# Performance work log

Measured on AMD Instinct MI355X. Metric: run time of the kernel, lower is better.

The kernel has to match this reference:

```python
import jax, jax.numpy as jnp
import numpy as np

L = 96   # num_layers per GRU stack == seq_len (required by h0 construction in source)
B = 128  # batch
T = 96   # seq_len
D = 3    # input features (x,y,z landmark coords)


def _u(key, shape, s):
    return jax.random.uniform(key, shape, jnp.float32, minval=-s, maxval=s)


def setup_inputs() -> dict:
    key = jax.random.key(0)
    ks = iter(jax.random.split(key, 40))
    inp = {"x": jax.random.normal(next(ks), (B, T, D), jnp.float32)}

    def gru_params(pfx, din, h):
        s = 1.0 / np.sqrt(h).astype(np.float32)  # PyTorch GRU init scale
        inp[pfx + "_wih0"] = _u(next(ks), (3 * h, din), s)   # layer 0 input weights
        inp[pfx + "_bih0"] = _u(next(ks), (3 * h,), s)
        inp[pfx + "_whh0"] = _u(next(ks), (3 * h, h), s)
        inp[pfx + "_bhh0"] = _u(next(ks), (3 * h,), s)
        inp[pfx + "_wih"] = _u(next(ks), (L - 1, 3 * h, h), s)  # layers 1..L-1 (input dim == h)
        inp[pfx + "_bih"] = _u(next(ks), (L - 1, 3 * h), s)
        inp[pfx + "_whh"] = _u(next(ks), (L - 1, 3 * h, h), s)
        inp[pfx + "_bhh"] = _u(next(ks), (L - 1, 3 * h), s)

    gru_params("g1", D, 64)
    gru_params("g2", 64, 128)
    gru_params("g3", 128, 64)

    inp["d1_w"] = _u(next(ks), (64, 64), 1.0 / 8)
    inp["d1_b"] = _u(next(ks), (64,), 1.0 / 8)
    inp["d2_w"] = _u(next(ks), (32, 64), 1.0 / 8)
    inp["d2_b"] = _u(next(ks), (32,), 1.0 / 8)
    inp["d3_w"] = _u(next(ks), (250, 32), 1.0 / np.sqrt(32).astype(np.float32))
    inp["d3_b"] = _u(next(ks), (250,), 1.0 / np.sqrt(32).astype(np.float32))
    return inp


def _gru_layer(x, wih, bih, whh, bhh):
    # x: [B,T,Din]; wih: [3H,Din]; whh: [3H,H]. PyTorch gate order: r,z,n.
    h = whh.shape[1]
    xg = jnp.einsum('btd,gd->btg', x, wih) + bih  # precompute input gates [B,T,3H]

    def step(hprev, xg_t):
        hg = hprev @ whh.T + bhh
        xr, xz, xn = jnp.split(xg_t, 3, axis=-1)
        hr, hz, hn = jnp.split(hg, 3, axis=-1)
        r = jax.nn.sigmoid(xr + hr)
        z = jax.nn.sigmoid(xz + hz)
        n = jnp.tanh(xn + r * hn)
        hnew = (1.0 - z) * n + z * hprev
        return hnew, hnew

    h0 = jnp.zeros((x.shape[0], h), x.dtype)
    _, ys = jax.lax.scan(step, h0, jnp.swapaxes(xg, 0, 1))  # scan over time
    return jnp.swapaxes(ys, 0, 1)  # [B,T,H]


def _gru_stack(x, wih0, bih0, whh0, bhh0, wih, bih, whh, bhh):
    y = _gru_layer(x, wih0, bih0, whh0, bhh0)

    def body(y, p):
        return _gru_layer(y, p[0], p[1], p[2], p[3]), None

    y, _ = jax.lax.scan(body, y, (wih, bih, whh, bhh))  # scan over layers 1..L-1
    return y


def reference(x,
              g1_wih0, g1_bih0, g1_whh0, g1_bhh0, g1_wih, g1_bih, g1_whh, g1_bhh,
              g2_wih0, g2_bih0, g2_whh0, g2_bhh0, g2_wih, g2_bih, g2_whh, g2_bhh,
              g3_wih0, g3_bih0, g3_whh0, g3_bhh0, g3_wih, g3_bih, g3_whh, g3_bhh,
              d1_w, d1_b, d2_w, d2_b, d3_w, d3_b):
    y = _gru_stack(x, g1_wih0, g1_bih0, g1_whh0, g1_bhh0, g1_wih, g1_bih, g1_whh, g1_bhh)
    y = _gru_stack(y, g2_wih0, g2_bih0, g2_whh0, g2_bhh0, g2_wih, g2_bih, g2_whh, g2_bhh)
    y = _gru_stack(y, g3_wih0, g3_bih0, g3_whh0, g3_bhh0, g3_wih, g3_bih, g3_whh, g3_bhh)
    h = y[:, -1, :]  # last timestep [B,64]
    h = jax.nn.relu(h @ d1_w.T + d1_b)
    h = jax.nn.relu(h @ d2_w.T + d2_b)
    return jax.nn.relu(h @ d3_w.T + d3_b)  # [B,250]
```

## Files before the change

kernel.cpp:

```cpp
#include <hip/hip_runtime.h>


#define TPB 512
#define DRING 4
#define FS 64
#define PROBE_A 0x51CAFE77
#define PROBE_B 0x2B2B2B2B

typedef float vf4 __attribute__((ext_vector_type(4)));

__device__ __forceinline__ float sigmoid_f(float x) { return 1.0f / (1.0f + __expf(-x)); }
__device__ __forceinline__ float tanh_f(float x)    { return 1.0f - 2.0f / (__expf(2.0f * x) + 1.0f); }

__device__ __forceinline__ int cp_load(const int* p) {
    return __hip_atomic_load(p, __ATOMIC_RELAXED, __HIP_MEMORY_SCOPE_AGENT);
}
__device__ __forceinline__ void cp_store(int* p, int v) {
    __hip_atomic_store(p, v, __ATOMIC_RELAXED, __HIP_MEMORY_SCOPE_AGENT);
}
__device__ __forceinline__ int cp_poll_nz(const int* p) {
    int v;
    while (!(v = cp_load(p))) __builtin_amdgcn_s_sleep(8);
    return v;
}

__device__ __forceinline__ void vmwait0() { asm volatile("s_waitcnt vmcnt(0)" ::: "memory"); }
__device__ __forceinline__ int ld_l2_b32_wait(const int* p) {
    int r;
    asm volatile("global_load_dword %0, %1, off sc0\n\t"
                 "s_waitcnt vmcnt(0)"
                 : "=v"(r) : "v"(p) : "memory");
    return r;
}
__device__ __forceinline__ void st_l2_b32(int* p, int v) {
    asm volatile("global_store_dword %0, %1, off sc0" :: "v"(p), "v"(v) : "memory");
}
__device__ __forceinline__ void st_l2_f4(float* p, float4 v) {
    vf4 w; w[0] = v.x; w[1] = v.y; w[2] = v.z; w[3] = v.w;
    asm volatile("global_store_dwordx4 %0, %1, off sc0" :: "v"(p), "v"(w) : "memory");
}
__device__ __forceinline__ void ld_l2_2xf4(const float* p0, const float* p1,
                                           vf4& a, vf4& b) {
    asm volatile("global_load_dwordx4 %0, %2, off sc0\n\t"
                 "global_load_dwordx4 %1, %3, off sc0\n\t"
                 "s_waitcnt vmcnt(0)"
                 : "=&v"(a), "=&v"(b)
                 : "v"(p0), "v"(p1)
                 : "memory");
}
__device__ __forceinline__ void ld_l2_4xf4(const float* p0, const float* p1,
                                           const float* p2, const float* p3,
                                           vf4& a, vf4& b, vf4& c, vf4& d) {
    asm volatile("global_load_dwordx4 %0, %4, off sc0\n\t"
                 "global_load_dwordx4 %1, %5, off sc0\n\t"
                 "global_load_dwordx4 %2, %6, off sc0\n\t"
                 "global_load_dwordx4 %3, %7, off sc0\n\t"
                 "s_waitcnt vmcnt(0)"
                 : "=&v"(a), "=&v"(b), "=&v"(c), "=&v"(d)
                 : "v"(p0), "v"(p1), "v"(p2), "v"(p3)
                 : "memory");
}

__device__ __forceinline__ void st_cp_f4(float* p, float4 v) {
    vf4 w; w[0] = v.x; w[1] = v.y; w[2] = v.z; w[3] = v.w;
    asm volatile("global_store_dwordx4 %0, %1, off sc0 sc1" :: "v"(p), "v"(w) : "memory");
}
__device__ __forceinline__ void ld_cp_2xf4(const float* p0, const float* p1,
                                           vf4& a, vf4& b) {
    asm volatile("global_load_dwordx4 %0, %2, off sc0 sc1\n\t"
                 "global_load_dwordx4 %1, %3, off sc0 sc1\n\t"
                 "s_waitcnt vmcnt(0)"
                 : "=&v"(a), "=&v"(b)
                 : "v"(p0), "v"(p1)
                 : "memory");
}
__device__ __forceinline__ void ld_cp_4xf4(const float* p0, const float* p1,
                                           const float* p2, const float* p3,
                                           vf4& a, vf4& b, vf4& c, vf4& d) {
    asm volatile("global_load_dwordx4 %0, %4, off sc0 sc1\n\t"
                 "global_load_dwordx4 %1, %5, off sc0 sc1\n\t"
                 "global_load_dwordx4 %2, %6, off sc0 sc1\n\t"
                 "global_load_dwordx4 %3, %7, off sc0 sc1\n\t"
                 "s_waitcnt vmcnt(0)"
                 : "=&v"(a), "=&v"(b), "=&v"(c), "=&v"(d)
                 : "v"(p0), "v"(p1), "v"(p2), "v"(p3)
                 : "memory");
}

__device__ __forceinline__ void wait_flag(int* fp, int tgt, bool fast) {
    if (fast) { while (ld_l2_b32_wait(fp) < tgt) __builtin_amdgcn_s_sleep(1); }
    else      { while (cp_load(fp) < tgt)        __builtin_amdgcn_s_sleep(2); }
}

struct PassArgs {
    const float* wih0; const float* bih0; const float* whh0; const float* bhh0;
    const float* wihA; const float* bihA; const float* whhA; const float* bhhA;
    int firstLayer;
    int NL;
    const float* seqIn;
    long seqTs;
    float* seqOut;
    float* hFinal;
    float* rings;
    int* done;
    int* prb;
    const float* xg;
};

template<int STACK>
__global__ __launch_bounds__(TPB, 2) void pass_kernel(PassArgs A)
{
    constexpr int NG    = (STACK == 2) ? 96 : 192;
    constexpr int NB    = (STACK == 2) ? 128 : 64;
    constexpr int KH    = (STACK == 2) ? 128 : 64;
    constexpr int KI    = (STACK == 2) ? 128 : 64;
    constexpr int PARTS = (STACK == 2) ? 4 : 2;
    constexpr int JS    = NG / 3;
    constexpr int NGG   = NG / 6;
    constexpr int BGN   = TPB / NGG;
    constexpr int WROW  = NGG * 12;
    constexpr int XGT   = (STACK == 2) ? 384 * 128 : 192 * 128;

    __shared__ __align__(16) float wt_hh[(KH / 2) * WROW];
    __shared__ __align__(16) float wt_ih[(KI / 2) * WROW];
    __shared__ __align__(16) float atile[64 * NB];
    __shared__ __align__(16) float hbuf[64 * 64];

    const int tid  = threadIdx.x;

    const int bidx = blockIdx.x;
    int l, part;
    if (STACK == 2) { l = 6  * (bidx & 7) + ((bidx >> 3) >> 2); part = (bidx >> 3) & 3; }
    else            { l = 12 * (bidx & 7) + ((bidx >> 3) >> 1); part = (bidx >> 3) & 1; }
    const int rb = l * PARTS + part;
    const int gl = A.firstLayer + l;

    const int gg = tid / BGN;
    const int bg = tid % BGN;
    const int jl0 = 2 * gg, jl1 = 2 * gg + 1;
    const int b0 = 4 * bg;

    const float *wih, *bih, *whh, *bhh;
    if (gl == 0) { wih = A.wih0; bih = A.bih0; whh = A.whh0; bhh = A.bhh0; }
    else {
        const int wsz = (STACK == 2) ? 384 * 128 : 192 * 64;
        const int bs  = (STACK == 2) ? 384 : 192;
        wih = A.wihA + (size_t)(gl - 1) * wsz; bih = A.bihA + (size_t)(gl - 1) * bs;
        whh = A.whhA + (size_t)(gl - 1) * wsz; bhh = A.bhhA + (size_t)(gl - 1) * bs;
    }

    auto grow = [&](int r) -> int {
        if (STACK == 2) return (r >> 5) * 128 + 32 * part + (r & 31);
        return r;
    };

    for (int i = tid; i < NG * KH; i += TPB) {
        int r = i / KH, k = i - r * KH;
        int g = r / JS, j = r - g * JS;
        wt_hh[(k >> 1) * WROW + (j >> 1) * 12 + (k & 1) * 6 + g * 2 + (j & 1)]
            = whh[(size_t)grow(r) * KH + k];
    }
    if (l > 0) {
        for (int i = tid; i < NG * KI; i += TPB) {
            int r = i / KI, k = i - r * KI;
            int g = r / JS, j = r - g * JS;
            wt_ih[(k >> 1) * WROW + (j >> 1) * 12 + (k & 1) * 6 + g * 2 + (j & 1)]
                = wih[(size_t)grow(r) * KI + k];
        }
    }

    float bR[2], bZ[2], bNH[2], bNI[2];
#pragma unroll
    for (int jj = 0; jj < 2; ++jj) {
        int jl = jl0 + jj;
        bR[jj]  = bhh[grow(jl)]          + bih[grow(jl)];
        bZ[jj]  = bhh[grow(JS + jl)]     + bih[grow(JS + jl)];
        bNH[jj] = bhh[grow(2 * JS + jl)];
        bNI[jj] = bih[grow(2 * JS + jl)];
    }

    float hprev[2][4];
#pragma unroll
    for (int jj = 0; jj < 2; ++jj)
#pragma unroll
        for (int bb = 0; bb < 4; ++bb) hprev[jj][bb] = 0.0f;

    bool f_in = false, f_out = false, f_fl_self = false, f_fl_par = false, f_fl_child = false;
    {
        int* hsk = (int*)atile;
        const int NL = A.NL;
        if (STACK != 2) {
            if (tid == 0 && l < NL - 1) {
                int* rg = A.prb + (size_t)rb * FS;
                cp_store(rg, PROBE_A); vmwait0();
                (void)ld_l2_b32_wait(rg);
                cp_store(rg, PROBE_B); vmwait0();
                cp_store(rg + 1, 1);
            }
            if (tid == 1 && l > 0) {
                int* rg = A.prb + (size_t)((l - 1) * PARTS + part) * FS;
                (void)cp_poll_nz(rg + 1);
                int v = ld_l2_b32_wait(rg);
                cp_store(rg + 2, (v == PROBE_A) ? 2 : 1);
            }
            if (tid >= 8 && tid < 12) {
                int j = l - 2 + (tid - 8);
                hsk[tid - 8] = (j >= 0 && j < NL - 1)
                    ? cp_poll_nz(A.prb + (size_t)(j * PARTS + part) * FS + 2) : 0;
            }
        } else {
            if (part == 0 && tid < 4 && (tid > 0 || l < NL - 1)) {
                int* rg = A.prb + (size_t)(l * 4 + tid) * FS;
                cp_store(rg, PROBE_A); vmwait0();
                (void)ld_l2_b32_wait(rg);
                cp_store(rg, PROBE_B); vmwait0();
                cp_store(rg + 1, 1);
            }
            if (tid == 4 && (part != 0 || l > 0)) {
                int* rg = (part != 0) ? A.prb + (size_t)(l * 4 + part) * FS
                                      : A.prb + (size_t)((l - 1) * 4) * FS;
                (void)cp_poll_nz(rg + 1);
                int v = ld_l2_b32_wait(rg);
                cp_store(rg + 2, (v == PROBE_A) ? 2 : 1);
            }
            if (tid >= 8 && tid < 28) {
                int q = tid - 8, r = q >> 2, p = q & 3;
                int a = l - 2 + r;
                bool valid = (a >= 0 && a < NL) && (p > 0 || a < NL - 1);
                hsk[q] = valid ? cp_poll_nz(A.prb + (size_t)(a * 4 + p) * FS + 2) : 0;
            }
        }
        __syncthreads();
        if (STACK != 2) {
            const int NLl = A.NL;
            bool pp0 = hsk[0] == 2, pp1 = hsk[1] == 2, pp2 = hsk[2] == 2, pp3 = hsk[3] == 2;
            f_in       = (l > 0) && pp1;
            f_out      = (l == NLl - 1) || pp2;
            f_fl_self  = (l == 0 || pp1) && (l == NLl - 1 || pp2);
            f_fl_par   = (l > 0) && pp1 && (l < 2 || pp0);
            f_fl_child = (l < NLl - 1) && pp2 && (l + 2 >= NLl || pp3);
        } else {
            const int NLl = A.NL;
            bool S[5], T[4];
#pragma unroll
            for (int r = 0; r < 5; ++r)
                S[r] = hsk[r * 4 + 1] == 2 && hsk[r * 4 + 2] == 2 && hsk[r * 4 + 3] == 2;
#pragma unroll
            for (int r = 0; r < 4; ++r) T[r] = hsk[r * 4 + 0] == 2;
            f_out      = S[2] && (l == NLl - 1 || (S[3] && T[2]));
            f_in       = (l > 0) && S[1] && S[2] && T[1];
            f_fl_self  = S[2] && (l == 0 || (S[1] && T[1])) && (l == NLl - 1 || (S[3] && T[2]));
            f_fl_par   = (l > 0) && S[1] && S[2] && T[1] && (l < 2 || (S[0] && T[0]));
            f_fl_child = (l < NLl - 1) && S[2] && S[3] && T[2] && (l + 2 >= NLl || (S[4] && T[3]));
        }
        __syncthreads();
    }

    auto gemmP = [&](const float* wt, const float* at, int astride,
                     float (&accR)[2][4], float (&accZ)[2][4], float (&accN)[2][4]) {
#pragma unroll 2
        for (int k2 = 0; k2 < 32; ++k2) {
            const float* wr = wt + k2 * WROW + gg * 12;
            vf4 q0 = *(const vf4*)(wr);
            vf4 q1 = *(const vf4*)(wr + 4);
            vf4 q2 = *(const vf4*)(wr + 8);
            const float* ar = at + (2 * k2) * astride + b0;
            float4 a0v = *(const float4*)(ar);
            float4 a1v = *(const float4*)(ar + astride);
            float a0[4] = {a0v.x, a0v.y, a0v.z, a0v.w};
            float a1[4] = {a1v.x, a1v.y, a1v.z, a1v.w};
#pragma unroll
            for (int bb = 0; bb < 4; ++bb) {
                accR[0][bb] += q0.x * a0[bb];  accR[1][bb] += q0.y * a0[bb];
                accZ[0][bb] += q0.z * a0[bb];  accZ[1][bb] += q0.w * a0[bb];
                accN[0][bb] += q1.x * a0[bb];  accN[1][bb] += q1.y * a0[bb];
                accR[0][bb] += q1.z * a1[bb];  accR[1][bb] += q1.w * a1[bb];
                accZ[0][bb] += q2.x * a1[bb];  accZ[1][bb] += q2.y * a1[bb];
                accN[0][bb] += q2.z * a1[bb];  accN[1][bb] += q2.w * a1[bb];
            }
        }
    };

    auto stage2 = [&](int baseBlk, int slotT, int kt, bool fast) {
        const float* p[4];
#pragma unroll
        for (int q = 0; q < 4; ++q) {
            int u4 = tid + q * TPB, r = u4 >> 5, c4 = u4 & 31, kk = kt * 64 + r;
            p[q] = A.rings + ((size_t)(baseBlk + (kk >> 5)) * DRING + slotT) * 4096
                           + (kk & 31) * 128 + 4 * c4;
        }
        vf4 ta, tb, tc, td;
        if (fast) ld_l2_4xf4(p[0], p[1], p[2], p[3], ta, tb, tc, td);
        else      ld_cp_4xf4(p[0], p[1], p[2], p[3], ta, tb, tc, td);
        {
            int u4, r, c4;
            u4 = tid;           r = u4 >> 5; c4 = u4 & 31; *(vf4*)&atile[r * 128 + 4 * c4] = ta;
            u4 = tid + TPB;     r = u4 >> 5; c4 = u4 & 31; *(vf4*)&atile[r * 128 + 4 * c4] = tb;
            u4 = tid + 2 * TPB; r = u4 >> 5; c4 = u4 & 31; *(vf4*)&atile[r * 128 + 4 * c4] = tc;
            u4 = tid + 3 * TPB; r = u4 >> 5; c4 = u4 & 31; *(vf4*)&atile[r * 128 + 4 * c4] = td;
        }
    };

    for (int t = 0; t < 96; ++t) {
        float accR[2][4] = {}, accZ[2][4] = {}, accNH[2][4] = {}, accNI[2][4] = {};

        if (STACK != 2) {
            if (t > 0) gemmP(wt_hh, hbuf, 64, accR, accZ, accNH);

            if (tid < 8) {
                int grp = tid >> 2, idx = tid & 3;
                int* fp = nullptr; int tgt = 0; bool fm = false;
                if (grp == 0) { if (l > 0 && idx == part)
                                { fp = &A.done[((l - 1) * PARTS + idx) * FS]; tgt = t + 1; fm = f_fl_par; } }
                else          { if (t >= DRING && l < A.NL - 1 && idx == part)
                                { fp = &A.done[((l + 1) * PARTS + idx) * FS]; tgt = t - DRING + 1; fm = f_fl_child; } }
                if (fp) wait_flag(fp, tgt, fm);
            }
            __syncthreads();

            if (l == 0) {
                const float* xgp = A.xg + (size_t)t * XGT + 64 * part + b0;
                auto xgacc = [&](int row, float (&acc)[4]) {
                    float4 xv = *(const float4*)&xgp[(size_t)row * 128];
                    acc[0] += xv.x; acc[1] += xv.y; acc[2] += xv.z; acc[3] += xv.w;
                };
                xgacc(jl0, accR[0]);            xgacc(jl1, accR[1]);
                xgacc(JS + jl0, accZ[0]);       xgacc(JS + jl1, accZ[1]);
                xgacc(2 * JS + jl0, accNI[0]);  xgacc(2 * JS + jl1, accNI[1]);
            } else {
                const float* slot = A.rings + ((size_t)((l - 1) * PARTS + part) * DRING + (t & 3)) * 4096;
                vf4 ta, tb;
                if (f_in) ld_l2_2xf4(slot + 4 * tid, slot + 4 * (tid + TPB), ta, tb);
                else      ld_cp_2xf4(slot + 4 * tid, slot + 4 * (tid + TPB), ta, tb);
                *(vf4*)&atile[4 * tid] = ta;
                *(vf4*)&atile[4 * (tid + TPB)] = tb;
                __syncthreads();
                gemmP(wt_ih, atile, 64, accR, accZ, accNI);
            }
        } else {
            if (t > 0) {
                if (tid < 4 && tid != part)
                    wait_flag(&A.done[(l * 4 + tid) * FS], t, f_fl_self);
                __syncthreads();
                for (int kt = 0; kt < 2; ++kt) {
                    if (kt) __syncthreads();
                    stage2(l * 4, (t - 1) & 3, kt, f_out);
                    __syncthreads();
                    gemmP(wt_hh + kt * 32 * WROW, atile, 128, accR, accZ, accNH);
                }
            }

            if (tid < 8) {
                int grp = tid >> 2, idx = tid & 3;
                int* fp = nullptr; int tgt = 0; bool fm = false;
                if (grp == 0) { if (l > 0) { fp = &A.done[((l - 1) * 4 + idx) * FS]; tgt = t + 1; fm = f_fl_par; } }
                else          { if (t >= DRING && l < A.NL - 1)
                                { fp = &A.done[((l + 1) * 4 + idx) * FS]; tgt = t - DRING + 1; fm = f_fl_child; } }
                if (fp) wait_flag(fp, tgt, fm);
            }
            __syncthreads();

            if (l == 0) {
                const float* xgp = A.xg + (size_t)t * XGT + b0;
                auto xgacc = [&](int row, float (&acc)[4]) {
                    float4 xv = *(const float4*)&xgp[(size_t)row * 128];
                    acc[0] += xv.x; acc[1] += xv.y; acc[2] += xv.z; acc[3] += xv.w;
                };
                xgacc(grow(jl0), accR[0]);            xgacc(grow(jl1), accR[1]);
                xgacc(grow(JS + jl0), accZ[0]);       xgacc(grow(JS + jl1), accZ[1]);
                xgacc(grow(2 * JS + jl0), accNI[0]);  xgacc(grow(2 * JS + jl1), accNI[1]);
            } else {
                for (int kt = 0; kt < 2; ++kt) {
                    if (kt) __syncthreads();
                    stage2((l - 1) * 4, t & 3, kt, f_in);
                    __syncthreads();
                    gemmP(wt_ih + kt * 32 * WROW, atile, 128, accR, accZ, accNI);
                }
            }
        }

        float4 hv[2];
#pragma unroll
        for (int jj = 0; jj < 2; ++jj) {
            float* hp = (float*)&hv[jj];
#pragma unroll
            for (int bb = 0; bb < 4; ++bb) {
                float r = sigmoid_f(accR[jj][bb] + bR[jj]);
                float z = sigmoid_f(accZ[jj][bb] + bZ[jj]);
                float n = tanh_f(accNI[jj][bb] + bNI[jj] + r * (accNH[jj][bb] + bNH[jj]));
                float h = (1.0f - z) * n + z * hprev[jj][bb];
                hprev[jj][bb] = h;
                hp[bb] = h;
            }
        }
        float* slot = A.rings + ((size_t)rb * DRING + (t & 3)) * 4096;
        if (STACK == 2) {
            if (f_out) {
                st_l2_f4(&slot[jl0 * 128 + b0], hv[0]);
                st_l2_f4(&slot[jl1 * 128 + b0], hv[1]);
            } else {
                st_cp_f4(&slot[jl0 * 128 + b0], hv[0]);
                st_cp_f4(&slot[jl1 * 128 + b0], hv[1]);
            }
            if (A.seqOut && l == A.NL - 1) {
                *(float4*)&A.seqOut[(size_t)t * 16384 + (32 * part + jl0) * 128 + b0] = hv[0];
                *(float4*)&A.seqOut[(size_t)t * 16384 + (32 * part + jl1) * 128 + b0] = hv[1];
            }
        } else {
            if (f_out) {
                st_l2_f4(&slot[jl0 * 64 + b0], hv[0]);
                st_l2_f4(&slot[jl1 * 64 + b0], hv[1]);
            } else {
                st_cp_f4(&slot[jl0 * 64 + b0], hv[0]);
                st_cp_f4(&slot[jl1 * 64 + b0], hv[1]);
            }
            *(float4*)&hbuf[jl0 * 64 + b0] = hv[0];
            *(float4*)&hbuf[jl1 * 64 + b0] = hv[1];
            if (A.seqOut && l == A.NL - 1) {
                *(float4*)&A.seqOut[(size_t)t * 16384 + jl0 * 128 + 64 * part + b0] = hv[0];
                *(float4*)&A.seqOut[(size_t)t * 16384 + jl1 * 128 + 64 * part + b0] = hv[1];
            }
            if (STACK == 3 && l == A.NL - 1 && t == 95 && A.hFinal) {
                *(float4*)&A.hFinal[jl0 * 128 + 64 * part + b0] = hv[0];
                *(float4*)&A.hFinal[jl1 * 128 + 64 * part + b0] = hv[1];
            }
        }
        vmwait0();
        __syncthreads();
        if (tid == 0) {
            if (f_fl_self) st_l2_b32(&A.done[rb * FS], t + 1);
            else           cp_store(&A.done[rb * FS], t + 1);
        }
    }
}

__global__ __launch_bounds__(256) void xg_kernel(const float* __restrict__ W,
    const float* __restrict__ X, float* __restrict__ XG,
    int NGtot, int din, long xts)
{
    __shared__ float xs[16384];
    const int t = blockIdx.x, r0 = blockIdx.y * 64, tid = threadIdx.x;
    for (int i = tid; i < din * 128; i += 256)
        xs[i] = X[(size_t)t * xts + i];
    __syncthreads();
    const int rr = tid >> 2, bq = tid & 3;
    const int r = r0 + rr;
    vf4 acc[8];
#pragma unroll
    for (int j = 0; j < 8; ++j) acc[j] = (vf4){0.f, 0.f, 0.f, 0.f};
    for (int k = 0; k < din; ++k) {
        float w = W[(size_t)r * din + k];
        const float* xr = &xs[k * 128 + bq * 32];
#pragma unroll
        for (int j = 0; j < 8; ++j) {
            vf4 xv = *(const vf4*)(xr + 4 * j);
            acc[j] += w * xv;
        }
    }
    float* out = &XG[((size_t)t * NGtot + r) * 128 + bq * 32];
#pragma unroll
    for (int j = 0; j < 8; ++j) *(vf4*)(out + 4 * j) = acc[j];
}

__global__ void xprep_kernel(const float* __restrict__ x, float* __restrict__ seqA)
{
    int i = blockIdx.x * 256 + threadIdx.x;
    if (i < 128 * 96 * 3) {
        int b = i / 288, r = i - b * 288;
        int t = r / 3, k = r - 3 * t;
        seqA[(size_t)t * 8192 + k * 128 + b] = x[i];
    }
}

__global__ __launch_bounds__(256) void head_kernel(
    const float* __restrict__ hF,
    const float* __restrict__ d1w, const float* __restrict__ d1b,
    const float* __restrict__ d2w, const float* __restrict__ d2b,
    const float* __restrict__ d3w, const float* __restrict__ d3b,
    float* __restrict__ out)
{
    const int b = blockIdx.x, tid = threadIdx.x;
    __shared__ float h1[64], h2[32];
    if (tid < 64) {
        float s = d1b[tid];
        for (int k = 0; k < 64; ++k) s += d1w[tid * 64 + k] * hF[k * 128 + b];
        h1[tid] = fmaxf(s, 0.0f);
    }
    __syncthreads();
    if (tid < 32) {
        float s = d2b[tid];
        for (int k = 0; k < 64; ++k) s += d2w[tid * 64 + k] * h1[k];
        h2[tid] = fmaxf(s, 0.0f);
    }
    __syncthreads();
    if (tid < 250) {
        float s = d3b[tid];
        for (int k = 0; k < 32; ++k) s += d3w[tid * 32 + k] * h2[k];
        out[b * 250 + tid] = fmaxf(s, 0.0f);
    }
}

extern "C" void kernel_launch(void* const* d_in, const int* in_sizes, int n_in,
                              void* d_out, int out_size, void* d_ws, size_t ws_size,
                              hipStream_t stream)
{
    const float* x       = (const float*)d_in[0];
    const float* g1_wih0 = (const float*)d_in[1];  const float* g1_bih0 = (const float*)d_in[2];
    const float* g1_whh0 = (const float*)d_in[3];  const float* g1_bhh0 = (const float*)d_in[4];
    const float* g1_wih  = (const float*)d_in[5];  const float* g1_bih  = (const float*)d_in[6];
    const float* g1_whh  = (const float*)d_in[7];  const float* g1_bhh  = (const float*)d_in[8];
    const float* g2_wih0 = (const float*)d_in[9];  const float* g2_bih0 = (const float*)d_in[10];
    const float* g2_whh0 = (const float*)d_in[11]; const float* g2_bhh0 = (const float*)d_in[12];
    const float* g2_wih  = (const float*)d_in[13]; const float* g2_bih  = (const float*)d_in[14];
    const float* g2_whh  = (const float*)d_in[15]; const float* g2_bhh  = (const float*)d_in[16];
    const float* g3_wih0 = (const float*)d_in[17]; const float* g3_bih0 = (const float*)d_in[18];
    const float* g3_whh0 = (const float*)d_in[19]; const float* g3_bhh0 = (const float*)d_in[20];
    const float* g3_wih  = (const float*)d_in[21]; const float* g3_bih  = (const float*)d_in[22];
    const float* g3_whh  = (const float*)d_in[23]; const float* g3_bhh  = (const float*)d_in[24];
    const float* d1w = (const float*)d_in[25]; const float* d1b = (const float*)d_in[26];
    const float* d2w = (const float*)d_in[27]; const float* d2b = (const float*)d_in[28];
    const float* d3w = (const float*)d_in[29]; const float* d3b = (const float*)d_in[30];

    float* wsf = (float*)d_ws;
    const size_t RINGS = (size_t)192 * DRING * 4096;
    const size_t B1SZ  = (size_t)96 * 128 * 128;
    const size_t SEQA  = (size_t)96 * 64 * 128;
    const int    SLOTN = 192 * FS;
    float* rings  = wsf;
    float* B1     = rings + RINGS;
    float* B2     = B1 + B1SZ;
    float* seqA   = B2 + B1SZ;
    float* hFinal = seqA + SEQA;
    int*   flags  = (int*)(hFinal + 8192);
    int*   prb    = flags + (size_t)4 * SLOTN;
    float* XG     = (float*)(prb + (size_t)4 * SLOTN);

    size_t zero_bytes = (B1SZ * 2 + SEQA + 8192) * sizeof(float)
                      + (size_t)8 * SLOTN * sizeof(int);
    (void)hipMemsetAsync(B1, 0, zero_bytes, stream);

    xprep_kernel<<<dim3(144), dim3(256), 0, stream>>>(x, seqA);

    PassArgs P;
    xg_kernel<<<dim3(96, 3), dim3(256), 0, stream>>>(g1_wih0, seqA, XG, 192, 3, 8192);
    P = {g1_wih0, g1_bih0, g1_whh0, g1_bhh0, g1_wih, g1_bih, g1_whh, g1_bhh,
         0, 96, seqA, 8192, B1, nullptr, rings, flags + 0 * SLOTN, prb + 0 * SLOTN, XG};
    pass_kernel<1><<<dim3(192), dim3(TPB), 0, stream>>>(P);

    xg_kernel<<<dim3(96, 6), dim3(256), 0, stream>>>(g2_wih0, B1, XG, 384, 64, 16384);
    P = {g2_wih0, g2_bih0, g2_whh0, g2_bhh0, g2_wih, g2_bih, g2_whh, g2_bhh,
         0, 48, B1, 16384, B2, nullptr, rings, flags + 1 * SLOTN, prb + 1 * SLOTN, XG};
    pass_kernel<2><<<dim3(192), dim3(TPB), 0, stream>>>(P);

    xg_kernel<<<dim3(96, 6), dim3(256), 0, stream>>>(g2_wih + (size_t)47 * 384 * 128, B2, XG,
                                                     384, 128, 16384);
    P = {g2_wih0, g2_bih0, g2_whh0, g2_bhh0, g2_wih, g2_bih, g2_whh, g2_bhh,
         48, 48, B2, 16384, B1, nullptr, rings, flags + 2 * SLOTN, prb + 2 * SLOTN, XG};
    pass_kernel<2><<<dim3(192), dim3(TPB), 0, stream>>>(P);

    xg_kernel<<<dim3(96, 3), dim3(256), 0, stream>>>(g3_wih0, B1, XG, 192, 128, 16384);
    P = {g3_wih0, g3_bih0, g3_whh0, g3_bhh0, g3_wih, g3_bih, g3_whh, g3_bhh,
         0, 96, B1, 16384, nullptr, hFinal, rings, flags + 3 * SLOTN, prb + 3 * SLOTN, XG};
    pass_kernel<3><<<dim3(192), dim3(TPB), 0, stream>>>(P);

    head_kernel<<<dim3(128), dim3(256), 0, stream>>>(hFinal, d1w, d1b, d2w, d2b, d3w, d3b,
                                                     (float*)d_out);
}
```

Measured before the change: 9.176 ms.

## Fuse first three GRU passes into one persistent kernel with cross-pass flag waits

Merges the stack-1 pass and both halves of the stack-2 pass into a single persistent kernel. The first layer of each later pass spins on the previous pass's per-timestep done flags instead of waiting for a kernel boundary, so the passes can overlap in a wavefront. The precomputed input-gate xg kernels for those passes are dropped, and the layer-0 input projection is computed in-kernel from the streamed sequence output. It uses separate ring buffers per pass, coherent stores for sequence outputs, and a larger shared-memory footprint. The risk is occupancy loss and deadlock if blocks of different phases are not co-resident.

Measured after the change: 8.108 ms. 11.6% less time.

```diff
diff --git a/kernel.cpp b/kernel.cpp
--- a/kernel.cpp
+++ b/kernel.cpp
@@ -105,13 +105,17 @@
     int* done;
     int* prb;
     const float* xg;
+    const int* prevDone;
+    int prevBase;
+    int prevN;
+    int cpSeqOut;
 };
 
 template<int STACK>
-__global__ __launch_bounds__(TPB, 2) void pass_kernel(PassArgs A)
+__device__ void pass_body(const PassArgs& A, int l, int part, int tid,
+                          float* wt_hh, float* wt_ih, float* atile, float* hbuf)
 {
     constexpr int NG    = (STACK == 2) ? 96 : 192;
-    constexpr int NB    = (STACK == 2) ? 128 : 64;
     constexpr int KH    = (STACK == 2) ? 128 : 64;
     constexpr int KI    = (STACK == 2) ? 128 : 64;
     constexpr int PARTS = (STACK == 2) ? 4 : 2;
@@ -121,19 +125,9 @@
     constexpr int WROW  = NGG * 12;
     constexpr int XGT   = (STACK == 2) ? 384 * 128 : 192 * 128;
 
-    __shared__ __align__(16) float wt_hh[(KH / 2) * WROW];
-    __shared__ __align__(16) float wt_ih[(KI / 2) * WROW];
-    __shared__ __align__(16) float atile[64 * NB];
-    __shared__ __align__(16) float hbuf[64 * 64];
-
-    const int tid  = threadIdx.x;
-
-    const int bidx = blockIdx.x;
-    int l, part;
-    if (STACK == 2) { l = 6  * (bidx & 7) + ((bidx >> 3) >> 2); part = (bidx >> 3) & 3; }
-    else            { l = 12 * (bidx & 7) + ((bidx >> 3) >> 1); part = (bidx >> 3) & 1; }
     const int rb = l * PARTS + part;
     const int gl = A.firstLayer + l;
+    const bool useXG = (A.xg != nullptr);
 
     const int gg = tid / BGN;
     const int bg = tid % BGN;
@@ -148,6 +142,8 @@
         wih = A.wihA + (size_t)(gl - 1) * wsz; bih = A.bihA + (size_t)(gl - 1) * bs;
         whh = A.whhA + (size_t)(gl - 1) * wsz; bhh = A.bhhA + (size_t)(gl - 1) * bs;
     }
+    const int din = (gl == 0) ? ((STACK == 1) ? 3 : ((STACK == 2) ? 64 : 128))
+                              : ((STACK == 2) ? 128 : 64);
 
     auto grow = [&](int r) -> int {
         if (STACK == 2) return (r >> 5) * 128 + 32 * part + (r & 31);
@@ -160,12 +156,12 @@
         wt_hh[(k >> 1) * WROW + (j >> 1) * 12 + (k & 1) * 6 + g * 2 + (j & 1)]
             = whh[(size_t)grow(r) * KH + k];
     }
-    if (l > 0) {
+    if (l > 0 || !useXG) {
         for (int i = tid; i < NG * KI; i += TPB) {
             int r = i / KI, k = i - r * KI;
             int g = r / JS, j = r - g * JS;
             wt_ih[(k >> 1) * WROW + (j >> 1) * 12 + (k & 1) * 6 + g * 2 + (j & 1)]
-                = wih[(size_t)grow(r) * KI + k];
+                = (k < din) ? wih[(size_t)grow(r) * din + k] : 0.0f;
         }
     }
 
@@ -353,14 +349,18 @@
             if (tid < 8) {
                 int grp = tid >> 2, idx = tid & 3;
                 int* fp = nullptr; int tgt = 0; bool fm = false;
-                if (grp == 0) { if (l > 0) { fp = &A.done[((l - 1) * 4 + idx) * FS]; tgt = t + 1; fm = f_fl_par; } }
-                else          { if (t >= DRING && l < A.NL - 1)
-                                { fp = &A.done[((l + 1) * 4 + idx) * FS]; tgt = t - DRING + 1; fm = f_fl_child; } }
+                if (grp == 0) {
+                    if (l > 0) { fp = &A.done[((l - 1) * 4 + idx) * FS]; tgt = t + 1; fm = f_fl_par; }
+                    else if (A.prevDone && idx < A.prevN)
+                         { fp = (int*)&A.prevDone[(A.prevBase + idx) * FS]; tgt = t + 1; fm = false; }
+                }
+                else { if (t >= DRING && l < A.NL - 1)
+                       { fp = &A.done[((l + 1) * 4 + idx) * FS]; tgt = t - DRING + 1; fm = f_fl_child; } }
                 if (fp) wait_flag(fp, tgt, fm);
             }
             __syncthreads();
 
-            if (l == 0) {
+            if (l == 0 && useXG) {
                 const float* xgp = A.xg + (size_t)t * XGT + b0;
                 auto xgacc = [&](int row, float (&acc)[4]) {
                     float4 xv = *(const float4*)&xgp[(size_t)row * 128];
@@ -370,9 +370,27 @@
                 xgacc(grow(JS + jl0), accZ[0]);       xgacc(grow(JS + jl1), accZ[1]);
                 xgacc(grow(2 * JS + jl0), accNI[0]);  xgacc(grow(2 * JS + jl1), accNI[1]);
             } else {
-                for (int kt = 0; kt < 2; ++kt) {
+                const int nkt = (l == 0 && A.firstLayer == 0) ? 1 : 2;
+                for (int kt = 0; kt < nkt; ++kt) {
                     if (kt) __syncthreads();
-                    stage2((l - 1) * 4, t & 3, kt, f_in);
+                    if (l == 0) {
+                        const float* src = A.seqIn + (size_t)t * A.seqTs + (size_t)kt * 64 * 128;
+                        if (A.prevDone) {
+                            vf4 a, b, c, d;
+                            ld_cp_4xf4(src + 4 * tid, src + 4 * (tid + TPB),
+                                       src + 4 * (tid + 2 * TPB), src + 4 * (tid + 3 * TPB),
+                                       a, b, c, d);
+                            *(vf4*)&atile[4 * tid] = a;
+                            *(vf4*)&atile[4 * (tid + TPB)] = b;
+                            *(vf4*)&atile[4 * (tid + 2 * TPB)] = c;
+                            *(vf4*)&atile[4 * (tid + 3 * TPB)] = d;
+                        } else {
+                            for (int i = tid; i < 2048; i += TPB)
+                                *(float4*)&atile[4 * i] = *(const float4*)(src + 4 * i);
+                        }
+                    } else {
+                        stage2((l - 1) * 4, t & 3, kt, f_in);
+                    }
                     __syncthreads();
                     gemmP(wt_ih + kt * 32 * WROW, atile, 128, accR, accZ, accNI);
                 }
@@ -403,8 +421,10 @@
                 st_cp_f4(&slot[jl1 * 128 + b0], hv[1]);
             }
             if (A.seqOut && l == A.NL - 1) {
-                *(float4*)&A.seqOut[(size_t)t * 16384 + (32 * part + jl0) * 128 + b0] = hv[0];
-                *(float4*)&A.seqOut[(size_t)t * 16384 + (32 * part + jl1) * 128 + b0] = hv[1];
+                float* o0 = &A.seqOut[(size_t)t * 16384 + (32 * part + jl0) * 128 + b0];
+                float* o1 = &A.seqOut[(size_t)t * 16384 + (32 * part + jl1) * 128 + b0];
+                if (A.cpSeqOut) { st_cp_f4(o0, hv[0]); st_cp_f4(o1, hv[1]); }
+                else            { *(float4*)o0 = hv[0]; *(float4*)o1 = hv[1]; }
             }
         } else {
             if (f_out) {
@@ -417,8 +437,10 @@
             *(float4*)&hbuf[jl0 * 64 + b0] = hv[0];
             *(float4*)&hbuf[jl1 * 64 + b0] = hv[1];
             if (A.seqOut && l == A.NL - 1) {
-                *(float4*)&A.seqOut[(size_t)t * 16384 + jl0 * 128 + 64 * part + b0] = hv[0];
-                *(float4*)&A.seqOut[(size_t)t * 16384 + jl1 * 128 + 64 * part + b0] = hv[1];
+                float* o0 = &A.seqOut[(size_t)t * 16384 + jl0 * 128 + 64 * part + b0];
+                float* o1 = &A.seqOut[(size_t)t * 16384 + jl1 * 128 + 64 * part + b0];
+                if (A.cpSeqOut) { st_cp_f4(o0, hv[0]); st_cp_f4(o1, hv[1]); }
+                else            { *(float4*)o0 = hv[0]; *(float4*)o1 = hv[1]; }
             }
             if (STACK == 3 && l == A.NL - 1 && t == 95 && A.hFinal) {
                 *(float4*)&A.hFinal[jl0 * 128 + 64 * part + b0] = hv[0];
@@ -432,6 +454,42 @@
             else           cp_store(&A.done[rb * FS], t + 1);
         }
     }
+}
+
+__global__ __launch_bounds__(TPB, 2) void fused_kernel(PassArgs P1, PassArgs P2, PassArgs P3)
+{
+    __shared__ __align__(16) float wt_hh[12288];
+    __shared__ __align__(16) float wt_ih[12288];
+    __shared__ __align__(16) float atile[8192];
+    __shared__ __align__(16) float hbuf[4096];
+
+    const int tid  = threadIdx.x;
+    const int bidx = blockIdx.x;
+
+    {
+        int l = 12 * (bidx & 7) + ((bidx >> 3) >> 1), part = (bidx >> 3) & 1;
+        pass_body<1>(P1, l, part, tid, wt_hh, wt_ih, atile, hbuf);
+    }
+    __syncthreads();
+    {
+        int l = 6 * (bidx & 7) + ((bidx >> 3) >> 2), part = (bidx >> 3) & 3;
+        pass_body<2>(P2, l, part, tid, wt_hh, wt_ih, atile, hbuf);
+        __syncthreads();
+        pass_body<2>(P3, l, part, tid, wt_hh, wt_ih, atile, hbuf);
+    }
+}
+
+__global__ __launch_bounds__(TPB, 2) void pass4_kernel(PassArgs A)
+{
+    __shared__ __align__(16) float wt_hh[12288];
+    __shared__ __align__(16) float wt_ih[12288];
+    __shared__ __align__(16) float atile[4096];
+    __shared__ __align__(16) float hbuf[4096];
+
+    const int tid  = threadIdx.x;
+    const int bidx = blockIdx.x;
+    int l = 12 * (bidx & 7) + ((bidx >> 3) >> 1), part = (bidx >> 3) & 1;
+    pass_body<3>(A, l, part, tid, wt_hh, wt_ih, atile, hbuf);
 }
 
 __global__ __launch_bounds__(256) void xg_kernel(const float* __restrict__ W,
@@ -526,8 +584,10 @@
     const size_t B1SZ  = (size_t)96 * 128 * 128;
     const size_t SEQA  = (size_t)96 * 64 * 128;
     const int    SLOTN = 192 * FS;
-    float* rings  = wsf;
-    float* B1     = rings + RINGS;
+    float* rings1 = wsf;
+    float* rings2 = rings1 + RINGS;
+    float* rings3 = rings2 + RINGS;
+    float* B1     = rings3 + RINGS;
     float* B2     = B1 + B1SZ;
     float* seqA   = B2 + B1SZ;
     float* hFinal = seqA + SEQA;
@@ -541,27 +601,25 @@
 
     xprep_kernel<<<dim3(144), dim3(256), 0, stream>>>(x, seqA);
 
-    PassArgs P;
     xg_kernel<<<dim3(96, 3), dim3(256), 0, stream>>>(g1_wih0, seqA, XG, 192, 3, 8192);
-    P = {g1_wih0, g1_bih0, g1_whh0, g1_bhh0, g1_wih, g1_bih, g1_whh, g1_bhh,
-         0, 96, seqA, 8192, B1, nullptr, rings, flags + 0 * SLOTN, prb + 0 * SLOTN, XG};
-    pass_kernel<1><<<dim3(192), dim3(TPB), 0, stream>>>(P);
-
-    xg_kernel<<<dim3(96, 6), dim3(256), 0, stream>>>(g2_wih0, B1, XG, 384, 64, 16384);
-    P = {g2_wih0, g2_bih0, g2_whh0, g2_bhh0, g2_wih, g2_bih, g2_whh, g2_bhh,
-         0, 48, B1, 16384, B2, nullptr, rings, flags + 1 * SLOTN, prb + 1 * SLOTN, XG};
-    pass_kernel<2><<<dim3(192), dim3(TPB), 0, stream>>>(P);
-
-    xg_kernel<<<dim3(96, 6), dim3(256), 0, stream>>>(g2_wih + (size_t)47 * 384 * 128, B2, XG,
-                                                     384, 128, 16384);
-    P = {g2_wih0, g2_bih0, g2_whh0, g2_bhh0, g2_wih, g2_bih, g2_whh, g2_bhh,
-         48, 48, B2, 16384, B1, nullptr, rings, flags + 2 * SLOTN, prb + 2 * SLOTN, XG};
-    pass_kernel<2><<<dim3(192), dim3(TPB), 0, stream>>>(P);
+
+    PassArgs P1 = {g1_wih0, g1_bih0, g1_whh0, g1_bhh0, g1_wih, g1_bih, g1_whh, g1_bhh,
+                   0, 96, seqA, 8192, B1, nullptr, rings1, flags + 0 * SLOTN, prb + 0 * SLOTN,
+                   XG, nullptr, 0, 0, 1};
+    PassArgs P2 = {g2_wih0, g2_bih0, g2_whh0, g2_bhh0, g2_wih, g2_bih, g2_whh, g2_bhh,
+                   0, 48, B1, 16384, B2, nullptr, rings2, flags + 1 * SLOTN, prb + 1 * SLOTN,
+                   nullptr, flags + 0 * SLOTN, 95 * 2, 2, 1};
+    PassArgs P3 = {g2_wih0, g2_bih0, g2_whh0, g2_bhh0, g2_wih, g2_bih, g2_whh, g2_bhh,
+                   48, 48, B2, 16384, B1, nullptr, rings3, flags + 2 * SLOTN, prb + 2 * SLOTN,
+                   nullptr, flags + 1 * SLOTN, 47 * 4, 4, 0};
+    fused_kernel<<<dim3(192), dim3(TPB), 0, stream>>>(P1, P2, P3);
 
     xg_kernel<<<dim3(96, 3), dim3(256), 0, stream>>>(g3_wih0, B1, XG, 192, 128, 16384);
-    P = {g3_wih0, g3_bih0, g3_whh0, g3_bhh0, g3_wih, g3_bih, g3_whh, g3_bhh,
-         0, 96, B1, 16384, nullptr, hFinal, rings, flags + 3 * SLOTN, prb + 3 * SLOTN, XG};
-    pass_kernel<3><<<dim3(192), dim3(TPB), 0, stream>>>(P);
+
+    PassArgs P4 = {g3_wih0, g3_bih0, g3_whh0, g3_bhh0, g3_wih, g3_bih, g3_whh, g3_bhh,
+                   0, 96, B1, 16384, nullptr, hFinal, rings1, flags + 3 * SLOTN, prb + 3 * SLOTN,
+                   XG, nullptr, 0, 0, 0};
+    pass4_kernel<<<dim3(192), dim3(TPB), 0, stream>>>(P4);
 
     head_kernel<<<dim3(128), dim3(256), 0, stream>>>(hFinal, d1w, d1b, d2w, d2b, d3w, d3b,
                                                      (float*)d_out);
```
